# Kernel optimization log

Hardware: AMD Instinct MI355X
Metric: run time of the kernel (lower is better)

Reference implementation:

```python
import jax, jax.numpy as jnp
import numpy as np

N = 50000
IN_DIM = 64
HID = [64, 64]
HEADS = 4
E0 = 800000
MLP_HID = 200
N_CLASSES = 2
NEG_SLOPE = 0.2
BN_EPS = 1e-5


def setup_inputs() -> dict:
    key = jax.random.key(0)
    ks = jax.random.split(key, 16)
    features = jax.random.normal(ks[0], (N, IN_DIM), dtype=jnp.float32)
    edge_index = jax.random.randint(ks[1], (2, E0), 0, N, dtype=jnp.int32)
    s = 0.05
    # GATConv layer 1 params
    W1 = jax.random.normal(ks[2], (IN_DIM, HEADS * HID[0]), dtype=jnp.float32) * s
    al1 = jax.random.normal(ks[3], (HEADS, HID[0]), dtype=jnp.float32) * s
    ar1 = jax.random.normal(ks[4], (HEADS, HID[0]), dtype=jnp.float32) * s
    b1 = jnp.zeros((HEADS * HID[0],), dtype=jnp.float32)
    # GATConv layer 2 params
    W2 = jax.random.normal(ks[5], (HID[0], HEADS * HID[1]), dtype=jnp.float32) * s
    al2 = jax.random.normal(ks[6], (HEADS, HID[1]), dtype=jnp.float32) * s
    ar2 = jax.random.normal(ks[7], (HEADS, HID[1]), dtype=jnp.float32) * s
    b2 = jnp.zeros((HEADS * HID[1],), dtype=jnp.float32)
    # MLP predictor: Linear(64->200), ReLU, BatchNorm1d(200), Linear(200->2)
    mw1 = jax.random.normal(ks[8], (HID[1], MLP_HID), dtype=jnp.float32) * s
    mb1 = jnp.zeros((MLP_HID,), dtype=jnp.float32)
    bn_g = jnp.ones((MLP_HID,), dtype=jnp.float32)
    bn_b = jnp.zeros((MLP_HID,), dtype=jnp.float32)
    mw2 = jax.random.normal(ks[9], (MLP_HID, N_CLASSES), dtype=jnp.float32) * s
    mb2 = jnp.zeros((N_CLASSES,), dtype=jnp.float32)
    return {"features": features, "edge_index": edge_index,
            "W1": W1, "al1": al1, "ar1": ar1, "b1": b1,
            "W2": W2, "al2": al2, "ar2": ar2, "b2": b2,
            "mw1": mw1, "mb1": mb1, "bn_g": bn_g, "bn_b": bn_b,
            "mw2": mw2, "mb2": mb2}


def _gat_layer(h, src, dst, W, al, ar, bias):
    # h: [N, F_in]; src/dst: [E] int (messages flow src -> dst, softmax over in-edges)
    H, D = al.shape
    feat = (h @ W).reshape(N, H, D)               # [N,H,D]
    el = jnp.sum(feat * al, axis=-1)              # [N,H]
    er = jnp.sum(feat * ar, axis=-1)              # [N,H]
    e = jax.nn.leaky_relu(el[src] + er[dst], NEG_SLOPE)  # [E,H]
    # numerically stable edge softmax segmented by dst
    m = jax.ops.segment_max(e, dst, num_segments=N)      # [N,H]
    ex = jnp.exp(e - m[dst])
    denom = jax.ops.segment_sum(ex, dst, num_segments=N)  # [N,H]
    a = ex / denom[dst]                                  # [E,H]
    msg = feat[src] * a[:, :, None]                      # [E,H,D]
    rst = jax.ops.segment_sum(msg, dst, num_segments=N)  # [N,H,D]
    rst = rst + bias.reshape(H, D)
    return jax.nn.relu(rst)


def reference(features, edge_index, W1, al1, ar1, b1, W2, al2, ar2, b2,
              mw1, mb1, bn_g, bn_b, mw2, mb2):
    # dgl.add_self_loop
    loop = jnp.arange(N, dtype=edge_index.dtype)
    src = jnp.concatenate([edge_index[0], loop])
    dst = jnp.concatenate([edge_index[1], loop])
    h = features
    h = _gat_layer(h, src, dst, W1, al1, ar1, b1).mean(axis=1)  # [N, 64]
    h = _gat_layer(h, src, dst, W2, al2, ar2, b2).mean(axis=1)  # [N, 64]
    # MLP predictor (dropout = identity in eval): Linear -> ReLU -> BatchNorm1d -> Linear
    z = jax.nn.relu(h @ mw1 + mb1)                       # [N, 200]
    mu = z.mean(axis=0)
    var = z.var(axis=0)                                  # biased var (batch stats)
    z = (z - mu) * jax.lax.rsqrt(var + BN_EPS) * bn_g + bn_b
    return z @ mw2 + mb2                                 # [N, 2]
```

## Files before the change

kernel.cpp:

```cpp
#include <hip/hip_runtime.h>
#include <hip/hip_bf16.h>

#define N_NODES 50000
#define E0_EDGES 800000
#define E_TOTAL 850000
#define NEG_SLOPE 0.2f
#define BN_EPS 1e-5f
#define CAP 64

typedef __attribute__((ext_vector_type(8))) short bf16x8;
typedef __attribute__((ext_vector_type(4))) float f32x4;

__device__ __forceinline__ float lrelu(float x) { return x > 0.f ? x : NEG_SLOPE * x; }

__device__ __forceinline__ ushort f2bf(float x) {
    __hip_bfloat16 b = __float2bfloat16(x);
    return *reinterpret_cast<ushort*>(&b);
}
__device__ __forceinline__ float bf2f(ushort u) {
    return __uint_as_float(((unsigned int)u) << 16);
}

__global__ void k_zero(int* __restrict__ deg, float* __restrict__ gsum, float* __restrict__ gsumsq) {
    int i = blockIdx.x * 256 + threadIdx.x;
    if (i < N_NODES) deg[i] = 0;
    if (i < 200) { gsum[i] = 0.f; gsumsq[i] = 0.f; }
}

__global__ void k_count(const int* __restrict__ ei, int* __restrict__ deg, int* __restrict__ rank) {
    int e = blockIdx.x * 256 + threadIdx.x;
    if (e >= E_TOTAL) return;
    int dst = (e < E0_EDGES) ? ei[E0_EDGES + e] : (e - E0_EDGES);
    rank[e] = atomicAdd(&deg[dst], 1);
}

__global__ void k_scanA(const int* __restrict__ deg, int* __restrict__ rowptr, int* __restrict__ bsum) {
    __shared__ int s[256];
    int i = blockIdx.x * 256 + threadIdx.x;
    int v = (i < N_NODES) ? deg[i] : 0;
    s[threadIdx.x] = v;
    __syncthreads();
    for (int off = 1; off < 256; off <<= 1) {
        int t = (threadIdx.x >= off) ? s[threadIdx.x - off] : 0;
        __syncthreads();
        s[threadIdx.x] += t;
        __syncthreads();
    }
    if (i < N_NODES) rowptr[i] = s[threadIdx.x];
    if (threadIdx.x == 255) bsum[blockIdx.x] = s[255];
}

__global__ void k_scanB(int* __restrict__ bsum, int nb) {
    __shared__ int s[256];
    int t = threadIdx.x;
    int v = (t < nb) ? bsum[t] : 0;
    s[t] = v;
    __syncthreads();
    for (int off = 1; off < 256; off <<= 1) {
        int u = (t >= off) ? s[t - off] : 0;
        __syncthreads();
        s[t] += u;
        __syncthreads();
    }
    if (t < nb) bsum[t] = s[t] - v;
}

__global__ void k_scanC(const int* __restrict__ deg, int* __restrict__ rowptr,
                        const int* __restrict__ bsum) {
    int i = blockIdx.x * 256 + threadIdx.x;
    if (i >= N_NODES) return;
    int rp = bsum[blockIdx.x] + rowptr[i] - deg[i];
    rowptr[i] = rp;
    if (i == N_NODES - 1) rowptr[N_NODES] = E_TOTAL;
}

__global__ void k_fill(const int* __restrict__ ei, const int* __restrict__ rowptr,
                       const int* __restrict__ rank, ushort* __restrict__ colidx) {
    int e = blockIdx.x * 256 + threadIdx.x;
    if (e >= E_TOTAL) return;
    int src, dst;
    if (e < E0_EDGES) { src = ei[e]; dst = ei[E0_EDGES + e]; }
    else { src = e - E0_EDGES; dst = src; }
    colidx[rowptr[dst] + rank[e]] = (ushort)src;
}

__global__ void k_wprep(const float* __restrict__ W1, const float* __restrict__ W2,
                        ushort* __restrict__ WbfT1, ushort* __restrict__ WbfT2) {
    int c = threadIdx.x;
    for (int k = 0; k < 64; k++) {
        WbfT1[c * 64 + k] = f2bf(W1[k * 256 + c]);
        WbfT2[c * 64 + k] = f2bf(W2[k * 256 + c]);
    }
}

__global__ void k_featprep(const float* __restrict__ x, ushort* __restrict__ xbf) {
    int i = (blockIdx.x * 256 + threadIdx.x) * 4;
    float4 v = *(const float4*)&x[i];
    ushort4 o;
    o.x = f2bf(v.x); o.y = f2bf(v.y); o.z = f2bf(v.z); o.w = f2bf(v.w);
    *(ushort4*)&xbf[i] = o;
}

__global__ void k_gemm_feat(const ushort* __restrict__ x, const ushort* __restrict__ WbfT,
                            const float* __restrict__ al, const float* __restrict__ ar,
                            ushort* __restrict__ featB, float* __restrict__ el, float* __restrict__ er) {
    __shared__ float fs[16][256];
    int tid = threadIdx.x;
    int wave = tid >> 6, lane = tid & 63;
    int row0 = blockIdx.x * 16;
    int lr = lane & 15;
    int q = lane >> 4;

    const ushort* ap = x + (size_t)(row0 + lr) * 64 + q * 8;
    bf16x8 a0 = *reinterpret_cast<const bf16x8*>(ap);
    bf16x8 a1 = *reinterpret_cast<const bf16x8*>(ap + 32);

#pragma unroll
    for (int t = 0; t < 4; t++) {
        int ct = wave * 4 + t;
        const ushort* wrow = WbfT + (size_t)(ct * 16 + lr) * 64 + q * 8;
        bf16x8 b0 = *reinterpret_cast<const bf16x8*>(wrow);
        bf16x8 b1 = *reinterpret_cast<const bf16x8*>(wrow + 32);
        f32x4 acc = {0.f, 0.f, 0.f, 0.f};
        acc = __builtin_amdgcn_mfma_f32_16x16x32_bf16(a0, b0, acc, 0, 0, 0);
        acc = __builtin_amdgcn_mfma_f32_16x16x32_bf16(a1, b1, acc, 0, 0, 0);
#pragma unroll
        for (int i = 0; i < 4; i++)
            fs[q * 4 + i][ct * 16 + lr] = acc[i];
    }
    __syncthreads();

    {
        int r = tid >> 4;
        int rem = tid & 15;
        int h = rem >> 2;
        int l = rem & 3;
        int d0 = l * 16;
        float vl = 0.f, vr = 0.f;
#pragma unroll
        for (int j = 0; j < 16; j += 4) {
            float4 f = *(const float4*)&fs[r][h * 64 + d0 + j];
            float4 a = *(const float4*)&al[h * 64 + d0 + j];
            float4 b = *(const float4*)&ar[h * 64 + d0 + j];
            vl += f.x * a.x + f.y * a.y + f.z * a.z + f.w * a.w;
            vr += f.x * b.x + f.y * b.y + f.z * b.z + f.w * b.w;
        }
        vl += __shfl_xor(vl, 1, 64); vl += __shfl_xor(vl, 2, 64);
        vr += __shfl_xor(vr, 1, 64); vr += __shfl_xor(vr, 2, 64);
        if (l == 0) {
            el[(row0 + r) * 4 + h] = vl;
            er[(row0 + r) * 4 + h] = vr;
        }
    }

    int c = tid;
    int srcc = ((c & 3) << 6) + (c >> 2);
#pragma unroll
    for (int r = 0; r < 16; r++)
        featB[(size_t)(row0 + r) * 256 + c] = f2bf(fs[r][srcc]);
}

__global__ void k_gat(const float4* __restrict__ el4, const float4* __restrict__ er4,
                      const int* __restrict__ rowptr, const ushort* __restrict__ colidx,
                      const ushort* __restrict__ featB, const float* __restrict__ bias,
                      ushort* __restrict__ hout) {
    __shared__ float4 sE[4][CAP];
    __shared__ int    sSrc[4][CAP];
    int tid = threadIdx.x;
    int w = tid >> 6, lane = tid & 63;
    int row = blockIdx.x * 4 + w;
    int start = rowptr[row];
    int deg = rowptr[row + 1] - start;
    int cached = min(deg, CAP);
    float4 erow = er4[row];

    float4 sm = make_float4(0.f, 0.f, 0.f, 0.f);
    for (int idx = lane; idx < cached; idx += 64) {
        int src = colidx[start + idx];
        float4 e = el4[src];
        float4 ex;
        ex.x = __expf(lrelu(e.x + erow.x));
        ex.y = __expf(lrelu(e.y + erow.y));
        ex.z = __expf(lrelu(e.z + erow.z));
        ex.w = __expf(lrelu(e.w + erow.w));
        sE[w][idx] = ex; sSrc[w][idx] = src;
        sm.x += ex.x; sm.y += ex.y; sm.z += ex.z; sm.w += ex.w;
    }
    for (int idx = CAP + lane; idx < deg; idx += 64) {
        int src = colidx[start + idx];
        float4 e = el4[src];
        sm.x += __expf(lrelu(e.x + erow.x));
        sm.y += __expf(lrelu(e.y + erow.y));
        sm.z += __expf(lrelu(e.z + erow.z));
        sm.w += __expf(lrelu(e.w + erow.w));
    }
#pragma unroll
    for (int off = 32; off; off >>= 1) {
        sm.x += __shfl_xor(sm.x, off, 64);
        sm.y += __shfl_xor(sm.y, off, 64);
        sm.z += __shfl_xor(sm.z, off, 64);
        sm.w += __shfl_xor(sm.w, off, 64);
    }
    float4 dr;
    dr.x = 1.f / sm.x; dr.y = 1.f / sm.y; dr.z = 1.f / sm.z; dr.w = 1.f / sm.w;

    const ushort4* featB4 = (const ushort4*)featB;
    float4 acc = make_float4(0.f, 0.f, 0.f, 0.f);
#pragma unroll 4
    for (int s = 0; s < cached; s++) {
        float4 ex = sE[w][s];
        int src = sSrc[w][s];
        ushort4 f = featB4[(size_t)src * 64 + lane];
        acc.x = fmaf(bf2f(f.x), ex.x, acc.x);
        acc.y = fmaf(bf2f(f.y), ex.y, acc.y);
        acc.z = fmaf(bf2f(f.z), ex.z, acc.z);
        acc.w = fmaf(bf2f(f.w), ex.w, acc.w);
    }
    for (int s = CAP; s < deg; s++) {
        int src = colidx[start + s];
        float4 e = el4[src];
        float4 ex;
        ex.x = __expf(lrelu(e.x + erow.x));
        ex.y = __expf(lrelu(e.y + erow.y));
        ex.z = __expf(lrelu(e.z + erow.z));
        ex.w = __expf(lrelu(e.w + erow.w));
        ushort4 f = featB4[(size_t)src * 64 + lane];
        acc.x = fmaf(bf2f(f.x), ex.x, acc.x);
        acc.y = fmaf(bf2f(f.y), ex.y, acc.y);
        acc.z = fmaf(bf2f(f.z), ex.z, acc.z);
        acc.w = fmaf(bf2f(f.w), ex.w, acc.w);
    }
    float o = fmaxf(fmaf(acc.x, dr.x, bias[lane]), 0.f)
            + fmaxf(fmaf(acc.y, dr.y, bias[64 + lane]), 0.f)
            + fmaxf(fmaf(acc.z, dr.z, bias[128 + lane]), 0.f)
            + fmaxf(fmaf(acc.w, dr.w, bias[192 + lane]), 0.f);
    hout[(size_t)row * 64 + lane] = f2bf(o * 0.25f);
}

#define MLP_BLOCKS 1250
#define MLP_CHUNKS 5
__global__ void k_mlp1_stats(const ushort* __restrict__ x, const float* __restrict__ W,
                             const float* __restrict__ b, ushort* __restrict__ z,
                             float* __restrict__ gsum, float* __restrict__ gsumsq) {
    __shared__ float xs[8][64];
    int tid = threadIdx.x;
    float bv = (tid < 200) ? b[tid] : 0.f;
    float s_ = 0.f, s2_ = 0.f;
    for (int chunk = 0; chunk < MLP_CHUNKS; chunk++) {
        int row0 = (blockIdx.x * MLP_CHUNKS + chunk) * 8;
        for (int i = tid; i < 512; i += 256)
            xs[i >> 6][i & 63] = bf2f(x[(size_t)(row0 + (i >> 6)) * 64 + (i & 63)]);
        __syncthreads();
        if (tid < 200) {
            float acc[8];
#pragma unroll
            for (int r = 0; r < 8; r++) acc[r] = 0.f;
            for (int k = 0; k < 64; k++) {
                float w = W[k * 200 + tid];
#pragma unroll
                for (int r = 0; r < 8; r++) acc[r] = fmaf(xs[r][k], w, acc[r]);
            }
#pragma unroll
            for (int r = 0; r < 8; r++) {
                float v = fmaxf(acc[r] + bv, 0.f);
                z[(size_t)(row0 + r) * 200 + tid] = f2bf(v);
                s_ += v;
                s2_ = fmaf(v, v, s2_);
            }
        }
        __syncthreads();
    }
    if (tid < 200) {
        atomicAdd(&gsum[tid], s_);
        atomicAdd(&gsumsq[tid], s2_);
    }
}

__global__ void k_bnprep(const float* __restrict__ gsum, const float* __restrict__ gsumsq,
                         const float* __restrict__ bn_g, const float* __restrict__ bn_b,
                         const float* __restrict__ mw2, const float* __restrict__ mb2,
                         float* __restrict__ w2p) {
    __shared__ float red0[256], red1[256];
    int c = threadIdx.x;
    float c0 = 0.f, c1 = 0.f;
    if (c < 200) {
        const float invN = 1.f / (float)N_NODES;
        float mu = gsum[c] * invN;
        float var = gsumsq[c] * invN - mu * mu;
        float alpha = bn_g[c] * rsqrtf(var + BN_EPS);
        float beta = bn_b[c] - mu * alpha;
        float w0 = mw2[c * 2], w1 = mw2[c * 2 + 1];
        w2p[c * 2] = alpha * w0;
        w2p[c * 2 + 1] = alpha * w1;
        c0 = beta * w0;
        c1 = beta * w1;
    }
    red0[c] = c0; red1[c] = c1;
    __syncthreads();
    for (int off = 128; off; off >>= 1) {
        if (c < off) { red0[c] += red0[c + off]; red1[c] += red1[c + off]; }
        __syncthreads();
    }
    if (c == 0) {
        w2p[400] = mb2[0] + red0[0];
        w2p[401] = mb2[1] + red1[0];
    }
}

__global__ void k_final(const ushort* __restrict__ z, const float* __restrict__ w2p, float* __restrict__ out) {
    int tid = threadIdx.x;
    int row = blockIdx.x * 4 + (tid >> 6);
    int lane = tid & 63;
    float a0 = 0.f, a1 = 0.f;
    for (int c = lane; c < 200; c += 64) {
        float v = bf2f(z[(size_t)row * 200 + c]);
        a0 = fmaf(v, w2p[c * 2], a0);
        a1 = fmaf(v, w2p[c * 2 + 1], a1);
    }
#pragma unroll
    for (int off = 32; off; off >>= 1) {
        a0 += __shfl_xor(a0, off, 64);
        a1 += __shfl_xor(a1, off, 64);
    }
    if (lane == 0) {
        out[row * 2] = a0 + w2p[400];
        out[row * 2 + 1] = a1 + w2p[401];
    }
}

extern "C" void kernel_launch(void* const* d_in, const int* in_sizes, int n_in,
                              void* d_out, int out_size, void* d_ws, size_t ws_size,
                              hipStream_t stream) {
    const float* features = (const float*)d_in[0];
    const int*   ei       = (const int*)d_in[1];
    const float* W1  = (const float*)d_in[2];
    const float* al1 = (const float*)d_in[3];
    const float* ar1 = (const float*)d_in[4];
    const float* b1  = (const float*)d_in[5];
    const float* W2  = (const float*)d_in[6];
    const float* al2 = (const float*)d_in[7];
    const float* ar2 = (const float*)d_in[8];
    const float* b2  = (const float*)d_in[9];
    const float* mw1 = (const float*)d_in[10];
    const float* mb1 = (const float*)d_in[11];
    const float* bng = (const float*)d_in[12];
    const float* bnb = (const float*)d_in[13];
    const float* mw2 = (const float*)d_in[14];
    const float* mb2 = (const float*)d_in[15];
    float* out = (float*)d_out;

    char* base = (char*)d_ws;
    size_t off = 0;
    auto alloc = [&](size_t bytes) -> char* {
        char* p = base + off;
        off = (off + bytes + 255) & ~(size_t)255;
        return p;
    };
    int*    deg    = (int*)alloc(N_NODES * 4);
    int*    rowptr = (int*)alloc((N_NODES + 1) * 4);
    int*    rank   = (int*)alloc(E_TOTAL * 4);
    int*    bsum   = (int*)alloc(256 * 4);
    ushort* colidx = (ushort*)alloc(E_TOTAL * 2);
    ushort* featB  = (ushort*)alloc((size_t)N_NODES * 256 * 2);
    float*  el     = (float*)alloc((size_t)N_NODES * 4 * 4);
    float*  er     = (float*)alloc((size_t)N_NODES * 4 * 4);
    ushort* xbf    = (ushort*)alloc((size_t)N_NODES * 64 * 2);
    ushort* h1     = (ushort*)alloc((size_t)N_NODES * 64 * 2);
    ushort* h2     = (ushort*)alloc((size_t)N_NODES * 64 * 2);
    ushort* z      = (ushort*)alloc((size_t)N_NODES * 200 * 2);
    float*  gsum   = (float*)alloc(256 * 4);
    float*  gsumsq = (float*)alloc(256 * 4);
    float*  w2p    = (float*)alloc(512 * 4);
    ushort* WbfT1  = (ushort*)alloc(256 * 64 * 2);
    ushort* WbfT2  = (ushort*)alloc(256 * 64 * 2);
    (void)ws_size; (void)in_sizes; (void)n_in; (void)out_size;

    const int NB_N = (N_NODES + 255) / 256;
    const int NB_E = (E_TOTAL + 255) / 256;

    k_zero<<<NB_N, 256, 0, stream>>>(deg, gsum, gsumsq);
    k_count<<<NB_E, 256, 0, stream>>>(ei, deg, rank);
    k_wprep<<<1, 256, 0, stream>>>(W1, W2, WbfT1, WbfT2);
    k_featprep<<<N_NODES * 64 / 1024, 256, 0, stream>>>(features, xbf);
    k_scanA<<<NB_N, 256, 0, stream>>>(deg, rowptr, bsum);
    k_scanB<<<1, 256, 0, stream>>>(bsum, NB_N);
    k_scanC<<<NB_N, 256, 0, stream>>>(deg, rowptr, bsum);
    k_fill<<<NB_E, 256, 0, stream>>>(ei, rowptr, rank, colidx);

    k_gemm_feat<<<N_NODES / 16, 256, 0, stream>>>(xbf, WbfT1, al1, ar1, featB, el, er);
    k_gat<<<N_NODES / 4, 256, 0, stream>>>((const float4*)el, (const float4*)er, rowptr, colidx, featB, b1, h1);

    k_gemm_feat<<<N_NODES / 16, 256, 0, stream>>>(h1, WbfT2, al2, ar2, featB, el, er);
    k_gat<<<N_NODES / 4, 256, 0, stream>>>((const float4*)el, (const float4*)er, rowptr, colidx, featB, b2, h2);

    k_mlp1_stats<<<MLP_BLOCKS, 256, 0, stream>>>(h2, mw1, mb1, z, gsum, gsumsq);
    k_bnprep<<<1, 256, 0, stream>>>(gsum, gsumsq, bng, bnb, mw2, mb2, w2p);
    k_final<<<N_NODES / 4, 256, 0, stream>>>(z, w2p, out);
}
```

Measured before the change: 320.2 us.

## Split GAT aggregation across half-waves with 16-byte loads; fuse prep kernels

The GAT aggregation loop now has each half-wave process alternate edges. Every lane loads 8 bf16 values (two dims times four heads) in one 16-byte load instead of 4 values, and the two halves' partial sums are combined with a cross-half shuffle before the bias, ReLU and head-mean epilogue. This halves the serial edge iterations per wave and widens the gathers, in exchange for extra accumulator registers and lanes idling on odd-degree nodes. Separately, the zero-init, weight transpose/convert and feature bf16 conversion kernels are merged into one launch. The weight transpose, which ran as a single block with a serial loop, is now spread over 256 blocks.

```diff
diff --git a/kernel.cpp b/kernel.cpp
--- a/kernel.cpp
+++ b/kernel.cpp
@@ -21,10 +21,30 @@
     return __uint_as_float(((unsigned int)u) << 16);
 }
 
-__global__ void k_zero(int* __restrict__ deg, float* __restrict__ gsum, float* __restrict__ gsumsq) {
-    int i = blockIdx.x * 256 + threadIdx.x;
-    if (i < N_NODES) deg[i] = 0;
-    if (i < 200) { gsum[i] = 0.f; gsumsq[i] = 0.f; }
+#define PREP_Z 196
+#define PREP_W 256
+#define PREP_F 3125
+__global__ void k_prep(int* __restrict__ deg, float* __restrict__ gsum, float* __restrict__ gsumsq,
+                       const float* __restrict__ W1, const float* __restrict__ W2,
+                       ushort* __restrict__ WbfT1, ushort* __restrict__ WbfT2,
+                       const float* __restrict__ x, ushort* __restrict__ xbf) {
+    int b = blockIdx.x;
+    int tid = threadIdx.x;
+    if (b < PREP_Z) {
+        int i = b * 256 + tid;
+        if (i < N_NODES) deg[i] = 0;
+        if (i < 200) { gsum[i] = 0.f; gsumsq[i] = 0.f; }
+    } else if (b < PREP_Z + PREP_W) {
+        int c = b - PREP_Z;
+        if (tid < 64)       WbfT1[c * 64 + tid] = f2bf(W1[tid * 256 + c]);
+        else if (tid < 128) WbfT2[c * 64 + (tid - 64)] = f2bf(W2[(tid - 64) * 256 + c]);
+    } else {
+        int i = ((b - PREP_Z - PREP_W) * 256 + tid) * 4;
+        float4 v = *(const float4*)&x[i];
+        ushort4 o;
+        o.x = f2bf(v.x); o.y = f2bf(v.y); o.z = f2bf(v.z); o.w = f2bf(v.w);
+        *(ushort4*)&xbf[i] = o;
+    }
 }
 
 __global__ void k_count(const int* __restrict__ ei, int* __restrict__ deg, int* __restrict__ rank) {
@@ -82,23 +102,6 @@
     if (e < E0_EDGES) { src = ei[e]; dst = ei[E0_EDGES + e]; }
     else { src = e - E0_EDGES; dst = src; }
     colidx[rowptr[dst] + rank[e]] = (ushort)src;
-}
-
-__global__ void k_wprep(const float* __restrict__ W1, const float* __restrict__ W2,
-                        ushort* __restrict__ WbfT1, ushort* __restrict__ WbfT2) {
-    int c = threadIdx.x;
-    for (int k = 0; k < 64; k++) {
-        WbfT1[c * 64 + k] = f2bf(W1[k * 256 + c]);
-        WbfT2[c * 64 + k] = f2bf(W2[k * 256 + c]);
-    }
-}
-
-__global__ void k_featprep(const float* __restrict__ x, ushort* __restrict__ xbf) {
-    int i = (blockIdx.x * 256 + threadIdx.x) * 4;
-    float4 v = *(const float4*)&x[i];
-    ushort4 o;
-    o.x = f2bf(v.x); o.y = f2bf(v.y); o.z = f2bf(v.z); o.w = f2bf(v.w);
-    *(ushort4*)&xbf[i] = o;
 }
 
 __global__ void k_gemm_feat(const ushort* __restrict__ x, const ushort* __restrict__ WbfT,
@@ -201,40 +204,60 @@
         sm.z += __shfl_xor(sm.z, off, 64);
         sm.w += __shfl_xor(sm.w, off, 64);
     }
-    float4 dr;
-    dr.x = 1.f / sm.x; dr.y = 1.f / sm.y; dr.z = 1.f / sm.z; dr.w = 1.f / sm.w;
-
-    const ushort4* featB4 = (const ushort4*)featB;
-    float4 acc = make_float4(0.f, 0.f, 0.f, 0.f);
-#pragma unroll 4
-    for (int s = 0; s < cached; s++) {
-        float4 ex = sE[w][s];
-        int src = sSrc[w][s];
-        ushort4 f = featB4[(size_t)src * 64 + lane];
-        acc.x = fmaf(bf2f(f.x), ex.x, acc.x);
-        acc.y = fmaf(bf2f(f.y), ex.y, acc.y);
-        acc.z = fmaf(bf2f(f.z), ex.z, acc.z);
-        acc.w = fmaf(bf2f(f.w), ex.w, acc.w);
-    }
-    for (int s = CAP; s < deg; s++) {
-        int src = colidx[start + s];
-        float4 e = el4[src];
-        float4 ex;
-        ex.x = __expf(lrelu(e.x + erow.x));
-        ex.y = __expf(lrelu(e.y + erow.y));
-        ex.z = __expf(lrelu(e.z + erow.z));
-        ex.w = __expf(lrelu(e.w + erow.w));
-        ushort4 f = featB4[(size_t)src * 64 + lane];
-        acc.x = fmaf(bf2f(f.x), ex.x, acc.x);
-        acc.y = fmaf(bf2f(f.y), ex.y, acc.y);
-        acc.z = fmaf(bf2f(f.z), ex.z, acc.z);
-        acc.w = fmaf(bf2f(f.w), ex.w, acc.w);
-    }
-    float o = fmaxf(fmaf(acc.x, dr.x, bias[lane]), 0.f)
-            + fmaxf(fmaf(acc.y, dr.y, bias[64 + lane]), 0.f)
-            + fmaxf(fmaf(acc.z, dr.z, bias[128 + lane]), 0.f)
-            + fmaxf(fmaf(acc.w, dr.w, bias[192 + lane]), 0.f);
-    hout[(size_t)row * 64 + lane] = f2bf(o * 0.25f);
+    float drv[4];
+    drv[0] = 1.f / sm.x; drv[1] = 1.f / sm.y; drv[2] = 1.f / sm.z; drv[3] = 1.f / sm.w;
+
+    int hl = lane >> 5;
+    int dl = lane & 31;
+    const bf16x8* fB8 = (const bf16x8*)featB;
+    float acc[8];
+#pragma unroll
+    for (int k = 0; k < 8; k++) acc[k] = 0.f;
+#pragma unroll 2
+    for (int s2 = 0; s2 * 2 < cached; s2++) {
+        int s = s2 * 2 + hl;
+        if (s < cached) {
+            float4 ex = sE[w][s];
+            int src = sSrc[w][s];
+            bf16x8 f = fB8[(size_t)src * 32 + dl];
+            float exv[4] = {ex.x, ex.y, ex.z, ex.w};
+#pragma unroll
+            for (int k = 0; k < 8; k++)
+                acc[k] = fmaf(bf2f((ushort)f[k]), exv[k & 3], acc[k]);
+        }
+    }
+    for (int s2 = 0; CAP + s2 * 2 < deg; s2++) {
+        int s = CAP + s2 * 2 + hl;
+        if (s < deg) {
+            int src = colidx[start + s];
+            float4 e = el4[src];
+            float exv[4];
+            exv[0] = __expf(lrelu(e.x + erow.x));
+            exv[1] = __expf(lrelu(e.y + erow.y));
+            exv[2] = __expf(lrelu(e.z + erow.z));
+            exv[3] = __expf(lrelu(e.w + erow.w));
+            bf16x8 f = fB8[(size_t)src * 32 + dl];
+#pragma unroll
+            for (int k = 0; k < 8; k++)
+                acc[k] = fmaf(bf2f((ushort)f[k]), exv[k & 3], acc[k]);
+        }
+    }
+#pragma unroll
+    for (int k = 0; k < 8; k++) acc[k] += __shfl_xor(acc[k], 32, 64);
+
+    int d0 = dl * 2;
+    float o0 = 0.f, o1 = 0.f;
+#pragma unroll
+    for (int h = 0; h < 4; h++) {
+        o0 += fmaxf(fmaf(acc[h],     drv[h], bias[h * 64 + d0]),     0.f);
+        o1 += fmaxf(fmaf(acc[4 + h], drv[h], bias[h * 64 + d0 + 1]), 0.f);
+    }
+    if (lane < 32) {
+        ushort2 o;
+        o.x = f2bf(o0 * 0.25f);
+        o.y = f2bf(o1 * 0.25f);
+        *(ushort2*)&hout[(size_t)row * 64 + d0] = o;
+    }
 }
 
 #define MLP_BLOCKS 1250
@@ -378,10 +401,10 @@
     const int NB_N = (N_NODES + 255) / 256;
     const int NB_E = (E_TOTAL + 255) / 256;
 
-    k_zero<<<NB_N, 256, 0, stream>>>(deg, gsum, gsumsq);
+    k_prep<<<PREP_Z + PREP_W + PREP_F, 256, 0, stream>>>(deg, gsum, gsumsq,
+                                                         W1, W2, WbfT1, WbfT2,
+                                                         features, xbf);
     k_count<<<NB_E, 256, 0, stream>>>(ei, deg, rank);
-    k_wprep<<<1, 256, 0, stream>>>(W1, W2, WbfT1, WbfT2);
-    k_featprep<<<N_NODES * 64 / 1024, 256, 0, stream>>>(features, xbf);
     k_scanA<<<NB_N, 256, 0, stream>>>(deg, rowptr, bsum);
     k_scanB<<<1, 256, 0, stream>>>(bsum, NB_N);
     k_scanC<<<NB_N, 256, 0, stream>>>(deg, rowptr, bsum);
```

Result: no change. 317.6 us (-0.8%).

## Merge preprocessing launches and fuse CSR fill with first feature GEMM

Applied to the files above, without the earlier changes.

Combines zeroing, weight transpose, and feature bf16 conversion into one multi-role kernel. Merges scanB into scanC by having each block reduce the preceding block sums itself. Runs the CSR fill and the first layer's feature GEMM as disjoint block ranges of a single launch. Stores per-edge rank as ushort to halve its traffic. The aim is fewer kernel launches and serialization gaps. The costs are redundant per-block reductions and the assumption that a node's in-degree fits in 16 bits.

```diff
diff --git a/kernel.cpp b/kernel.cpp
--- a/kernel.cpp
+++ b/kernel.cpp
@@ -21,17 +21,37 @@
     return __uint_as_float(((unsigned int)u) << 16);
 }
 
-__global__ void k_zero(int* __restrict__ deg, float* __restrict__ gsum, float* __restrict__ gsumsq) {
-    int i = blockIdx.x * 256 + threadIdx.x;
-    if (i < N_NODES) deg[i] = 0;
-    if (i < 200) { gsum[i] = 0.f; gsumsq[i] = 0.f; }
-}
-
-__global__ void k_count(const int* __restrict__ ei, int* __restrict__ deg, int* __restrict__ rank) {
+#define PREP_Z 196
+#define PREP_W 256
+#define PREP_F 3125
+__global__ void k_prep(int* __restrict__ deg, float* __restrict__ gsum, float* __restrict__ gsumsq,
+                       const float* __restrict__ W1, const float* __restrict__ W2,
+                       ushort* __restrict__ WbfT1, ushort* __restrict__ WbfT2,
+                       const float* __restrict__ x, ushort* __restrict__ xbf) {
+    int b = blockIdx.x;
+    int tid = threadIdx.x;
+    if (b < PREP_Z) {
+        int i = b * 256 + tid;
+        if (i < N_NODES) deg[i] = 0;
+        if (i < 200) { gsum[i] = 0.f; gsumsq[i] = 0.f; }
+    } else if (b < PREP_Z + PREP_W) {
+        int c = b - PREP_Z;
+        if (tid < 64)       WbfT1[c * 64 + tid] = f2bf(W1[tid * 256 + c]);
+        else if (tid < 128) WbfT2[c * 64 + (tid - 64)] = f2bf(W2[(tid - 64) * 256 + c]);
+    } else {
+        int i = ((b - PREP_Z - PREP_W) * 256 + tid) * 4;
+        float4 v = *(const float4*)&x[i];
+        ushort4 o;
+        o.x = f2bf(v.x); o.y = f2bf(v.y); o.z = f2bf(v.z); o.w = f2bf(v.w);
+        *(ushort4*)&xbf[i] = o;
+    }
+}
+
+__global__ void k_count(const int* __restrict__ ei, int* __restrict__ deg, ushort* __restrict__ rank) {
     int e = blockIdx.x * 256 + threadIdx.x;
     if (e >= E_TOTAL) return;
     int dst = (e < E0_EDGES) ? ei[E0_EDGES + e] : (e - E0_EDGES);
-    rank[e] = atomicAdd(&deg[dst], 1);
+    rank[e] = (ushort)atomicAdd(&deg[dst], 1);
 }
 
 __global__ void k_scanA(const int* __restrict__ deg, int* __restrict__ rowptr, int* __restrict__ bsum) {
@@ -50,64 +70,34 @@
     if (threadIdx.x == 255) bsum[blockIdx.x] = s[255];
 }
 
-__global__ void k_scanB(int* __restrict__ bsum, int nb) {
+__global__ void k_scanC(const int* __restrict__ deg, int* __restrict__ rowptr,
+                        const int* __restrict__ bsum, int nb) {
     __shared__ int s[256];
-    int t = threadIdx.x;
-    int v = (t < nb) ? bsum[t] : 0;
-    s[t] = v;
+    int tid = threadIdx.x;
+    s[tid] = (tid < nb && tid < blockIdx.x) ? bsum[tid] : 0;
     __syncthreads();
-    for (int off = 1; off < 256; off <<= 1) {
-        int u = (t >= off) ? s[t - off] : 0;
-        __syncthreads();
-        s[t] += u;
-        __syncthreads();
-    }
-    if (t < nb) bsum[t] = s[t] - v;
-}
-
-__global__ void k_scanC(const int* __restrict__ deg, int* __restrict__ rowptr,
-                        const int* __restrict__ bsum) {
-    int i = blockIdx.x * 256 + threadIdx.x;
+    for (int off = 128; off; off >>= 1) {
+        if (tid < off) s[tid] += s[tid + off];
+        __syncthreads();
+    }
+    int blockoff = s[0];
+    int i = blockIdx.x * 256 + tid;
     if (i >= N_NODES) return;
-    int rp = bsum[blockIdx.x] + rowptr[i] - deg[i];
-    rowptr[i] = rp;
+    rowptr[i] = blockoff + rowptr[i] - deg[i];
     if (i == N_NODES - 1) rowptr[N_NODES] = E_TOTAL;
 }
 
-__global__ void k_fill(const int* __restrict__ ei, const int* __restrict__ rowptr,
-                       const int* __restrict__ rank, ushort* __restrict__ colidx) {
-    int e = blockIdx.x * 256 + threadIdx.x;
-    if (e >= E_TOTAL) return;
-    int src, dst;
-    if (e < E0_EDGES) { src = ei[e]; dst = ei[E0_EDGES + e]; }
-    else { src = e - E0_EDGES; dst = src; }
-    colidx[rowptr[dst] + rank[e]] = (ushort)src;
-}
-
-__global__ void k_wprep(const float* __restrict__ W1, const float* __restrict__ W2,
-                        ushort* __restrict__ WbfT1, ushort* __restrict__ WbfT2) {
-    int c = threadIdx.x;
-    for (int k = 0; k < 64; k++) {
-        WbfT1[c * 64 + k] = f2bf(W1[k * 256 + c]);
-        WbfT2[c * 64 + k] = f2bf(W2[k * 256 + c]);
-    }
-}
-
-__global__ void k_featprep(const float* __restrict__ x, ushort* __restrict__ xbf) {
-    int i = (blockIdx.x * 256 + threadIdx.x) * 4;
-    float4 v = *(const float4*)&x[i];
-    ushort4 o;
-    o.x = f2bf(v.x); o.y = f2bf(v.y); o.z = f2bf(v.z); o.w = f2bf(v.w);
-    *(ushort4*)&xbf[i] = o;
-}
-
-__global__ void k_gemm_feat(const ushort* __restrict__ x, const ushort* __restrict__ WbfT,
-                            const float* __restrict__ al, const float* __restrict__ ar,
-                            ushort* __restrict__ featB, float* __restrict__ el, float* __restrict__ er) {
-    __shared__ float fs[16][256];
+#define FG_FILL 3321
+#define FG_GEMM 3125
+__device__ __forceinline__ void gemm_feat_body(int bid, const ushort* __restrict__ x,
+                                               const ushort* __restrict__ WbfT,
+                                               const float* __restrict__ al, const float* __restrict__ ar,
+                                               ushort* __restrict__ featB,
+                                               float* __restrict__ el, float* __restrict__ er,
+                                               float (*fs)[256]) {
     int tid = threadIdx.x;
     int wave = tid >> 6, lane = tid & 63;
-    int row0 = blockIdx.x * 16;
+    int row0 = bid * 16;
     int lr = lane & 15;
     int q = lane >> 4;
 
@@ -158,6 +148,31 @@
 #pragma unroll
     for (int r = 0; r < 16; r++)
         featB[(size_t)(row0 + r) * 256 + c] = f2bf(fs[r][srcc]);
+}
+
+__global__ void k_fill_gemm(const int* __restrict__ ei, const int* __restrict__ rowptr,
+                            const ushort* __restrict__ rank, ushort* __restrict__ colidx,
+                            const ushort* __restrict__ x, const ushort* __restrict__ WbfT,
+                            const float* __restrict__ al, const float* __restrict__ ar,
+                            ushort* __restrict__ featB, float* __restrict__ el, float* __restrict__ er) {
+    __shared__ float fs[16][256];
+    if (blockIdx.x < FG_FILL) {
+        int e = blockIdx.x * 256 + threadIdx.x;
+        if (e >= E_TOTAL) return;
+        int src, dst;
+        if (e < E0_EDGES) { src = ei[e]; dst = ei[E0_EDGES + e]; }
+        else { src = e - E0_EDGES; dst = src; }
+        colidx[rowptr[dst] + rank[e]] = (ushort)src;
+        return;
+    }
+    gemm_feat_body(blockIdx.x - FG_FILL, x, WbfT, al, ar, featB, el, er, fs);
+}
+
+__global__ void k_gemm_feat(const ushort* __restrict__ x, const ushort* __restrict__ WbfT,
+                            const float* __restrict__ al, const float* __restrict__ ar,
+                            ushort* __restrict__ featB, float* __restrict__ el, float* __restrict__ er) {
+    __shared__ float fs[16][256];
+    gemm_feat_body(blockIdx.x, x, WbfT, al, ar, featB, el, er, fs);
 }
 
 __global__ void k_gat(const float4* __restrict__ el4, const float4* __restrict__ er4,
@@ -358,7 +373,7 @@
     };
     int*    deg    = (int*)alloc(N_NODES * 4);
     int*    rowptr = (int*)alloc((N_NODES + 1) * 4);
-    int*    rank   = (int*)alloc(E_TOTAL * 4);
+    ushort* rank   = (ushort*)alloc(E_TOTAL * 2);
     int*    bsum   = (int*)alloc(256 * 4);
     ushort* colidx = (ushort*)alloc(E_TOTAL * 2);
     ushort* featB  = (ushort*)alloc((size_t)N_NODES * 256 * 2);
@@ -378,16 +393,15 @@
     const int NB_N = (N_NODES + 255) / 256;
     const int NB_E = (E_TOTAL + 255) / 256;
 
-    k_zero<<<NB_N, 256, 0, stream>>>(deg, gsum, gsumsq);
+    k_prep<<<PREP_Z + PREP_W + PREP_F, 256, 0, stream>>>(deg, gsum, gsumsq,
+                                                         W1, W2, WbfT1, WbfT2,
+                                                         features, xbf);
     k_count<<<NB_E, 256, 0, stream>>>(ei, deg, rank);
-    k_wprep<<<1, 256, 0, stream>>>(W1, W2, WbfT1, WbfT2);
-    k_featprep<<<N_NODES * 64 / 1024, 256, 0, stream>>>(features, xbf);
     k_scanA<<<NB_N, 256, 0, stream>>>(deg, rowptr, bsum);
-    k_scanB<<<1, 256, 0, stream>>>(bsum, NB_N);
-    k_scanC<<<NB_N, 256, 0, stream>>>(deg, rowptr, bsum);
-    k_fill<<<NB_E, 256, 0, stream>>>(ei, rowptr, rank, colidx);
-
-    k_gemm_feat<<<N_NODES / 16, 256, 0, stream>>>(xbf, WbfT1, al1, ar1, featB, el, er);
+    k_scanC<<<NB_N, 256, 0, stream>>>(deg, rowptr, bsum, NB_N);
+
+    k_fill_gemm<<<FG_FILL + FG_GEMM, 256, 0, stream>>>(ei, rowptr, rank, colidx,
+                                                       xbf, WbfT1, al1, ar1, featB, el, er);
     k_gat<<<N_NODES / 4, 256, 0, stream>>>((const float4*)el, (const float4*)er, rowptr, colidx, featB, b1, h1);
 
     k_gemm_feat<<<N_NODES / 16, 256, 0, stream>>>(h1, WbfT2, al2, ar2, featB, el, er);
```

Result: faster. 303.7 us (-5.1%).
